# Kernel tuning notes

Measured on AMD Instinct MI355X. Metric: run time of the kernel, lower is better.

Reference implementation:

```python
import jax, jax.numpy as jnp
import numpy as np

MASS = 1.0
CHARGE = 1.0
LX = 10.0
LY = 10.0
COUPLING = 1.0
NPER = 1  # module hardcodes self.nper = 1


def _periodic_internal_energy(xy):
    """Sum over 9 periodic image shifts of masked Coulomb energy.

    Mirrors MovingPoints.periodic_internal_energy / dislocated_internal_energy:
    for each (n, m) in {-1,0,1}^2, dists = cdist(xy, xy + [n*lx, m*ly]) with an
    +inf diagonal mask (so diagonal contributes 0 after 1/d), energy += sum(c*q^2/d).
    """
    n = xy.shape[0]
    eye = jnp.eye(n, dtype=bool)
    # pairwise coordinate differences, [N, N]
    dx = xy[:, None, 0] - xy[None, :, 0]
    dy = xy[:, None, 1] - xy[None, :, 1]
    cq2 = COUPLING * CHARGE ** 2
    energy = jnp.zeros((), dtype=xy.dtype)
    shifts = [(i * LX, j * LY) for i in range(-NPER, NPER + 1) for j in range(-NPER, NPER + 1)]
    for sx, sy in shifts:
        # cdist(xy, xy + shift): d_ij = ||xy_i - xy_j - shift||
        d2 = (dx - sx) ** 2 + (dy - sy) ** 2
        # diagonal masked with +inf in original -> 1/d = 0 on diagonal;
        # use where with a safe distance so forward is identical and grads are clean.
        d = jnp.sqrt(jnp.where(eye, 1.0, d2))
        energy = energy + jnp.sum(jnp.where(eye, 0.0, cq2 / d))
    return energy


def setup_inputs() -> dict:
    key = jax.random.key(0)
    k1, k2 = jax.random.split(key)
    N = 8192
    # positions uniform in the periodic box [0, LX] x [0, LY]
    xy = jax.random.uniform(k1, (N, 2), dtype=jnp.float32) * jnp.array([LX, LY], dtype=jnp.float32)
    pxy = jax.random.normal(k2, (N, 2), dtype=jnp.float32)
    return {"xy": xy, "pxy": pxy}


def reference(xy, pxy):
    # hamiltonian = kinetic_energy(pxy) + potential_energy_(xy) with no external objects
    ke = jnp.sum(pxy ** 2) / (2.0 * MASS)
    pe = _periodic_internal_energy(xy)
    return ke + pe
```

## Files before the change

### kernel.cpp

```cpp
#include <hip/hip_runtime.h>

#define N 8192

#define BGRID 64
#define BINV 6.4f
#define NBINS (BGRID * BGRID)
#define FDIM 127
#define FSIZE (FDIM * FDIM)
#define FH 0.15625f

#define RC2 0.25f
#define GA 3.75f
#define GB (-10.0f)
#define GC 12.0f

#define CELLG 20
#define CELLINV 2.0f
#define NCELLS (CELLG * CELLG)
#define CAP 64
#define SRCAP 384

#define FBLOCKS 64
#define HISTBLOCKS 4
#define KEBLOCKS 8
#define BUILDBLOCKS 8
#define NCORR 512

#define WS_F 0
#define WS_HIST 16384
#define WS_CELLN 32768
#define WS_CELLS 33280
#define WS_CORR 84480
#define WS_SR 84992
#define WS_KE 85504

#define RSQ __builtin_amdgcn_rsqf

__global__ __launch_bounds__(256) void prep_kernel(const float* __restrict__ xy,
                                                   const float* __restrict__ pxy,
                                                   float* __restrict__ F,
                                                   unsigned* __restrict__ hist,
                                                   float* __restrict__ ke_part,
                                                   unsigned* __restrict__ cell_n,
                                                   float2* __restrict__ cells) {
    const int t = threadIdx.x;
    const int b = blockIdx.x;
    if (b < FBLOCKS) {
        int k = b * 256 + t;
        if (k < FSIZE) {
            float a  = (float)(k % FDIM - 63) * FH;
            float bb = (float)(k / FDIM - 63) * FH;
            int ixm = (__builtin_fabsf(a)  <= 5.0f) ? 0 : (a  > 0.0f ? -1 : 1);
            int iym = (__builtin_fabsf(bb) <= 5.0f) ? 0 : (bb > 0.0f ? -1 : 1);
            float s = 0.0f;
            for (int iy = -1; iy <= 1; ++iy)
                for (int ix = -1; ix <= 1; ++ix) {
                    if (ix == ixm && iy == iym) continue;
                    float xs = __builtin_fmaf(10.0f, (float)ix, a);
                    float ys = __builtin_fmaf(10.0f, (float)iy, bb);
                    s += RSQ(xs * xs + ys * ys);
                }
            float ux = 5.0f - __builtin_fabsf(__builtin_fabsf(a) - 5.0f);
            float uy = 5.0f - __builtin_fabsf(__builtin_fabsf(bb) - 5.0f);
            float r2 = __builtin_fmaf(uy, uy, ux * ux);
            float gcap = (r2 >= RC2)
                       ? RSQ(r2)
                       : __builtin_fmaf(__builtin_fmaf(GC, r2, GB), r2, GA);
            F[k] = s + gcap;
        }
    } else if (b < FBLOCKS + HISTBLOCKS) {
        __shared__ unsigned lh[NBINS];
        const int hb = b - FBLOCKS;
        for (int k = t; k < NBINS; k += 256) lh[k] = 0u;
        __syncthreads();
        const float2* p2 = (const float2*)xy;
        for (int r = 0; r < 8; ++r) {
            float2 p = p2[hb * 2048 + r * 256 + t];
            int cx = (int)(p.x * BINV); cx = cx > 63 ? 63 : cx;
            int cy = (int)(p.y * BINV); cy = cy > 63 ? 63 : cy;
            atomicAdd(&lh[cy * BGRID + cx], 1u);
        }
        __syncthreads();
        for (int k = t; k < NBINS; k += 256) hist[hb * NBINS + k] = lh[k];
    } else if (b < FBLOCKS + HISTBLOCKS + KEBLOCKS) {
        const int kb = b - FBLOCKS - HISTBLOCKS;
        const float4* p4 = (const float4*)pxy;
        float acc = 0.0f;
        for (int k = kb * 256 + t; k < (2 * N) / 4; k += KEBLOCKS * 256) {
            float4 v = p4[k];
            acc += 0.5f * (v.x * v.x + v.y * v.y + v.z * v.z + v.w * v.w);
        }
        for (int off = 32; off > 0; off >>= 1)
            acc += __shfl_down(acc, off, 64);
        __shared__ float ws[4];
        if ((t & 63) == 0) ws[t >> 6] = acc;
        __syncthreads();
        if (t == 0) ke_part[kb] = (ws[0] + ws[1]) + (ws[2] + ws[3]);
    } else {
        const int pb = b - FBLOCKS - HISTBLOCKS - KEBLOCKS;
        const float2* p2 = (const float2*)xy;
        for (int k = pb * 1024 + t; k < pb * 1024 + 1024; k += 256) {
            float2 p = p2[k];
            int cx = (int)(p.x * CELLINV); cx = cx > CELLG - 1 ? CELLG - 1 : cx;
            int cy = (int)(p.y * CELLINV); cy = cy > CELLG - 1 ? CELLG - 1 : cy;
            int c = cy * CELLG + cx;
            unsigned slot = atomicAdd(&cell_n[c], 1u);
            if (slot < CAP) cells[c * CAP + slot] = p;
        }
    }
}

__global__ __launch_bounds__(128) void main_kernel(const float* __restrict__ F,
                                                   const unsigned* __restrict__ hist,
                                                   const unsigned* __restrict__ cell_n,
                                                   const float2* __restrict__ cells,
                                                   float* __restrict__ corr_part,
                                                   float* __restrict__ sr_part) {
    const int t = threadIdx.x;
    __shared__ float smem[1664];
    __shared__ float wsum[2];

    if (blockIdx.x < NCORR) {
        float (*corrF)[128] = (float (*)[128])smem;
        float (*corrN)[64]  = (float (*)[64])(smem + 1024);
        const int cid = blockIdx.x;
        const int y1 = cid >> 3;
        const int y2b = (cid & 7) * 8;
        const int x1 = t & 63;
        const int x2c = t >> 6;
        const int x2base = x2c * 32;
#pragma unroll
        for (int s = 0; s < 8; ++s) {
            if (t < FDIM)
                corrF[s][t] = F[(y1 - (y2b + s) + 63) * FDIM + t];
            if (t < 64) {
                int hi = (y2b + s) * BGRID + t;
                corrN[s][t] = (float)(hist[hi] + hist[NBINS + hi]
                                    + hist[2 * NBINS + hi] + hist[3 * NBINS + hi]);
            }
        }
        int h1 = y1 * BGRID + x1;
        float n1 = (float)(hist[h1] + hist[NBINS + h1]
                         + hist[2 * NBINS + h1] + hist[3 * NBINS + h1]);
        __syncthreads();
        const int fb = 63 + x1 - x2base;
        float acc = 0.0f;
#pragma unroll
        for (int s = 0; s < 8; ++s) {
            const float* Fr = &corrF[s][0];
            const float* Nr = &corrN[s][x2base];
            float sum = 0.0f;
#pragma unroll 8
            for (int k = 0; k < 32; ++k)
                sum = __builtin_fmaf(Nr[k], Fr[fb - k], sum);
            acc += sum;
        }
        acc *= n1;
        for (int off = 32; off > 0; off >>= 1)
            acc += __shfl_down(acc, off, 64);
        if ((t & 63) == 0) wsum[t >> 6] = acc;
        __syncthreads();
        if (t == 0) corr_part[cid] = wsum[0] + wsum[1];
        return;
    }

    float* spx  = smem;
    float* spy  = smem + 384;
    int*   stag = (int*)(smem + 768);

    const int c  = blockIdx.x - NCORR;
    const int cx = c % CELLG, cy = c / CELLG;

    const int offs[9][2] = {{0,0},{-1,-1},{0,-1},{1,-1},{-1,0},{1,0},{-1,1},{0,1},{1,1}};
    int base = 0, n0 = 0;
#pragma unroll
    for (int nn = 0; nn < 9; ++nn) {
        int cx2 = cx + offs[nn][0];
        cx2 += (cx2 < 0) ? CELLG : 0;  cx2 -= (cx2 >= CELLG) ? CELLG : 0;
        int cy2 = cy + offs[nn][1];
        cy2 += (cy2 < 0) ? CELLG : 0;  cy2 -= (cy2 >= CELLG) ? CELLG : 0;
        int cc = cy2 * CELLG + cx2;
        int len = (int)cell_n[cc];  len = len > CAP ? CAP : len;
        if (nn == 0) n0 = len;
        for (int k = t; k < len; k += 128) {
            int d = base + k;
            if (d < SRCAP) {
                float2 q = cells[cc * CAP + k];
                spx[d] = q.x;  spy[d] = q.y;  stag[d] = cc * CAP + k;
            }
        }
        base += len;
    }
    const int M = base > SRCAP ? SRCAP : base;
    __syncthreads();

    float acc = 0.0f;
    for (int i = 0; i < n0; ++i) {
        float pxi = spx[i], pyi = spy[i];
        int itag = c * CAP + i;
        for (int j = t; j < M; j += 128) {
            float dx = pxi - spx[j];
            float dy = pyi - spy[j];
            float ux = 5.0f - __builtin_fabsf(__builtin_fabsf(dx) - 5.0f);
            float uy = 5.0f - __builtin_fabsf(__builtin_fabsf(dy) - 5.0f);
            float s2 = __builtin_fmaf(uy, uy, ux * ux);
            float v = RSQ(s2) - __builtin_fmaf(__builtin_fmaf(GC, s2, GB), s2, GA);
            bool ok = (s2 < RC2) && (stag[j] != itag);
            acc += ok ? v : 0.0f;
        }
    }
    for (int off = 32; off > 0; off >>= 1)
        acc += __shfl_down(acc, off, 64);
    if ((t & 63) == 0) wsum[t >> 6] = acc;
    __syncthreads();
    if (t == 0) sr_part[c] = wsum[0] + wsum[1];
}

__global__ __launch_bounds__(1024) void finish_kernel(const float* __restrict__ corr_part,
                                                      const float* __restrict__ sr_part,
                                                      const float* __restrict__ ke_part,
                                                      const float* __restrict__ F,
                                                      float* __restrict__ out) {
    const int t = threadIdx.x;
    float acc = 0.0f;
    if (t < NCORR) acc += corr_part[t];
    if (t < NCELLS) acc += sr_part[t];
    if (t < KEBLOCKS) acc += ke_part[t];
    if (t == 0) acc -= (float)N * F[63 * FDIM + 63];
    for (int off = 32; off > 0; off >>= 1)
        acc += __shfl_down(acc, off, 64);
    __shared__ float ws[16];
    if ((t & 63) == 0) ws[t >> 6] = acc;
    __syncthreads();
    if (t == 0) {
        float s = 0.0f;
        for (int w = 0; w < 16; ++w) s += ws[w];
        out[0] = s;
    }
}

extern "C" void kernel_launch(void* const* d_in, const int* in_sizes, int n_in,
                              void* d_out, int out_size, void* d_ws, size_t ws_size,
                              hipStream_t stream) {
    const float* xy  = (const float*)d_in[0];
    const float* pxy = (const float*)d_in[1];
    float* out       = (float*)d_out;
    float* wsf       = (float*)d_ws;
    float* F         = wsf + WS_F;
    unsigned* hist   = (unsigned*)(wsf + WS_HIST);
    unsigned* cell_n = (unsigned*)(wsf + WS_CELLN);
    float2* cells    = (float2*)(wsf + WS_CELLS);
    float* corr_part = wsf + WS_CORR;
    float* sr_part   = wsf + WS_SR;
    float* ke_part   = wsf + WS_KE;

    hipMemsetAsync(cell_n, 0, NCELLS * sizeof(unsigned), stream);
    prep_kernel<<<FBLOCKS + HISTBLOCKS + KEBLOCKS + BUILDBLOCKS, 256, 0, stream>>>(
        xy, pxy, F, hist, ke_part, cell_n, cells);
    main_kernel<<<NCORR + NCELLS, 128, 0, stream>>>(
        F, hist, cell_n, cells, corr_part, sr_part);
    finish_kernel<<<1, 1024, 0, stream>>>(corr_part, sr_part, ke_part, F, out);
}
```

Before: 32.20 us.

## Build cell lists per slice in shared memory and drop the memset launch

The cell-binning step now gives each build block its own per-cell slice, counted with shared-memory atomics instead of global atomics. Per-slice counts are written to global memory, so the separate hipMemsetAsync that zeroed counters is no longer needed. The short-range blocks gather 72 segments through a prefix sum and a binary search, and take the self-exclusion tag from the stored source index. This removes one launch and global atomic contention, at the cost of more gather logic and a per-slice capacity of 24 that could overflow for dense cells.

```diff
diff --git a/kernel.cpp b/kernel.cpp
--- a/kernel.cpp
+++ b/kernel.cpp
@@ -17,22 +17,22 @@
 #define CELLG 20
 #define CELLINV 2.0f
 #define NCELLS (CELLG * CELLG)
-#define CAP 64
+#define NSLICE 8
+#define CAPS 24
 #define SRCAP 384
 
 #define FBLOCKS 64
 #define HISTBLOCKS 4
 #define KEBLOCKS 8
-#define BUILDBLOCKS 8
 #define NCORR 512
 
 #define WS_F 0
 #define WS_HIST 16384
-#define WS_CELLN 32768
-#define WS_CELLS 33280
-#define WS_CORR 84480
-#define WS_SR 84992
-#define WS_KE 85504
+#define WS_CNT 32768
+#define WS_CELLS 36864
+#define WS_CORR 190464
+#define WS_SR 190976
+#define WS_KE 191488
 
 #define RSQ __builtin_amdgcn_rsqf
 
@@ -41,7 +41,7 @@
                                                    float* __restrict__ F,
                                                    unsigned* __restrict__ hist,
                                                    float* __restrict__ ke_part,
-                                                   unsigned* __restrict__ cell_n,
+                                                   unsigned* __restrict__ cnt_g,
                                                    float2* __restrict__ cells) {
     const int t = threadIdx.x;
     const int b = blockIdx.x;
@@ -97,22 +97,27 @@
         __syncthreads();
         if (t == 0) ke_part[kb] = (ws[0] + ws[1]) + (ws[2] + ws[3]);
     } else {
+        __shared__ unsigned cur[NCELLS];
         const int pb = b - FBLOCKS - HISTBLOCKS - KEBLOCKS;
         const float2* p2 = (const float2*)xy;
-        for (int k = pb * 1024 + t; k < pb * 1024 + 1024; k += 256) {
-            float2 p = p2[k];
+        for (int k = t; k < NCELLS; k += 256) cur[k] = 0u;
+        __syncthreads();
+        for (int r = 0; r < 4; ++r) {
+            float2 p = p2[pb * 1024 + r * 256 + t];
             int cx = (int)(p.x * CELLINV); cx = cx > CELLG - 1 ? CELLG - 1 : cx;
             int cy = (int)(p.y * CELLINV); cy = cy > CELLG - 1 ? CELLG - 1 : cy;
             int c = cy * CELLG + cx;
-            unsigned slot = atomicAdd(&cell_n[c], 1u);
-            if (slot < CAP) cells[c * CAP + slot] = p;
-        }
+            unsigned slot = atomicAdd(&cur[c], 1u);
+            if (slot < CAPS) cells[(c * NSLICE + pb) * CAPS + slot] = p;
+        }
+        __syncthreads();
+        for (int k = t; k < NCELLS; k += 256) cnt_g[k * NSLICE + pb] = cur[k];
     }
 }
 
 __global__ __launch_bounds__(128) void main_kernel(const float* __restrict__ F,
                                                    const unsigned* __restrict__ hist,
-                                                   const unsigned* __restrict__ cell_n,
+                                                   const unsigned* __restrict__ cnt_g,
                                                    const float2* __restrict__ cells,
                                                    float* __restrict__ corr_part,
                                                    float* __restrict__ sr_part) {
@@ -164,40 +169,56 @@
         return;
     }
 
-    float* spx  = smem;
-    float* spy  = smem + 384;
-    int*   stag = (int*)(smem + 768);
+    float* spx      = smem;
+    float* spy      = smem + 384;
+    int*   stag     = (int*)(smem + 768);
+    int*   segbase  = (int*)(smem + 1152);
+    unsigned* seglen = (unsigned*)(smem + 1225);
+    int*   cc9      = (int*)(smem + 1297);
 
     const int c  = blockIdx.x - NCORR;
     const int cx = c % CELLG, cy = c / CELLG;
 
-    const int offs[9][2] = {{0,0},{-1,-1},{0,-1},{1,-1},{-1,0},{1,0},{-1,1},{0,1},{1,1}};
-    int base = 0, n0 = 0;
-#pragma unroll
-    for (int nn = 0; nn < 9; ++nn) {
-        int cx2 = cx + offs[nn][0];
+    if (t < 9) {
+        const int ox[9] = {0,-1,0,1,-1,1,-1,0,1};
+        const int oy[9] = {0,-1,-1,-1,0,0,1,1,1};
+        int cx2 = cx + ox[t];
         cx2 += (cx2 < 0) ? CELLG : 0;  cx2 -= (cx2 >= CELLG) ? CELLG : 0;
-        int cy2 = cy + offs[nn][1];
+        int cy2 = cy + oy[t];
         cy2 += (cy2 < 0) ? CELLG : 0;  cy2 -= (cy2 >= CELLG) ? CELLG : 0;
-        int cc = cy2 * CELLG + cx2;
-        int len = (int)cell_n[cc];  len = len > CAP ? CAP : len;
-        if (nn == 0) n0 = len;
-        for (int k = t; k < len; k += 128) {
-            int d = base + k;
-            if (d < SRCAP) {
-                float2 q = cells[cc * CAP + k];
-                spx[d] = q.x;  spy[d] = q.y;  stag[d] = cc * CAP + k;
-            }
-        }
-        base += len;
-    }
-    const int M = base > SRCAP ? SRCAP : base;
+        cc9[t] = cy2 * CELLG + cx2;
+    }
+    __syncthreads();
+    if (t < 72) {
+        unsigned L = cnt_g[cc9[t >> 3] * NSLICE + (t & 7)];
+        seglen[t] = L > CAPS ? CAPS : L;
+    }
+    __syncthreads();
+    if (t < 73) {
+        int b2 = 0;
+        for (int j = 0; j < t; ++j) b2 += (int)seglen[j];
+        segbase[t] = b2;
+    }
+    __syncthreads();
+    const int n0 = segbase[8];
+    int M = segbase[72];  M = M > SRCAP ? SRCAP : M;
+
+    for (int g = t; g < M; g += 128) {
+        int lo = 0, hi = 71;
+        while (lo < hi) {
+            int mid = (lo + hi + 1) >> 1;
+            if (segbase[mid] <= g) lo = mid; else hi = mid - 1;
+        }
+        int src = (cc9[lo >> 3] * NSLICE + (lo & 7)) * CAPS + (g - segbase[lo]);
+        float2 q = cells[src];
+        spx[g] = q.x;  spy[g] = q.y;  stag[g] = src;
+    }
     __syncthreads();
 
     float acc = 0.0f;
     for (int i = 0; i < n0; ++i) {
         float pxi = spx[i], pyi = spy[i];
-        int itag = c * CAP + i;
+        int itag = stag[i];
         for (int j = t; j < M; j += 128) {
             float dx = pxi - spx[j];
             float dy = pyi - spy[j];
@@ -248,16 +269,15 @@
     float* wsf       = (float*)d_ws;
     float* F         = wsf + WS_F;
     unsigned* hist   = (unsigned*)(wsf + WS_HIST);
-    unsigned* cell_n = (unsigned*)(wsf + WS_CELLN);
+    unsigned* cnt_g  = (unsigned*)(wsf + WS_CNT);
     float2* cells    = (float2*)(wsf + WS_CELLS);
     float* corr_part = wsf + WS_CORR;
     float* sr_part   = wsf + WS_SR;
     float* ke_part   = wsf + WS_KE;
 
-    hipMemsetAsync(cell_n, 0, NCELLS * sizeof(unsigned), stream);
-    prep_kernel<<<FBLOCKS + HISTBLOCKS + KEBLOCKS + BUILDBLOCKS, 256, 0, stream>>>(
-        xy, pxy, F, hist, ke_part, cell_n, cells);
+    prep_kernel<<<FBLOCKS + HISTBLOCKS + KEBLOCKS + NSLICE, 256, 0, stream>>>(
+        xy, pxy, F, hist, ke_part, cnt_g, cells);
     main_kernel<<<NCORR + NCELLS, 128, 0, stream>>>(
-        F, hist, cell_n, cells, corr_part, sr_part);
+        F, hist, cnt_g, cells, corr_part, sr_part);
     finish_kernel<<<1, 1024, 0, stream>>>(corr_part, sr_part, ke_part, F, out);
 }
```

Result: faster. 27.39 us (-14.9%).

## Fuse prep into main kernel with per-block redundant histogram and neighbor gather

Applied to the files above, without the earlier changes.

Removes the memset and prep kernel. Each correlation block now rebuilds the full 64x64 histogram in shared memory and computes its F rows inline, and each short-range block scans all points to gather its 3x3 neighborhood. Kinetic energy moves into the finish kernel. This trades two launches and global round-trips for much redundant work: 912 blocks each read all 8192 points and do shared atomics.

```diff
diff --git a/kernel.cpp b/kernel.cpp
--- a/kernel.cpp
+++ b/kernel.cpp
@@ -6,7 +6,6 @@
 #define BINV 6.4f
 #define NBINS (BGRID * BGRID)
 #define FDIM 127
-#define FSIZE (FDIM * FDIM)
 #define FH 0.15625f
 
 #define RC2 0.25f
@@ -17,138 +16,82 @@
 #define CELLG 20
 #define CELLINV 2.0f
 #define NCELLS (CELLG * CELLG)
-#define CAP 64
 #define SRCAP 384
 
-#define FBLOCKS 64
-#define HISTBLOCKS 4
-#define KEBLOCKS 8
-#define BUILDBLOCKS 8
 #define NCORR 512
-
-#define WS_F 0
-#define WS_HIST 16384
-#define WS_CELLN 32768
-#define WS_CELLS 33280
-#define WS_CORR 84480
-#define WS_SR 84992
-#define WS_KE 85504
+#define NBLK (NCORR + NCELLS)
+
+#define WS_CORR 0
+#define WS_SR 512
 
 #define RSQ __builtin_amdgcn_rsqf
 
-__global__ __launch_bounds__(256) void prep_kernel(const float* __restrict__ xy,
-                                                   const float* __restrict__ pxy,
-                                                   float* __restrict__ F,
-                                                   unsigned* __restrict__ hist,
-                                                   float* __restrict__ ke_part,
-                                                   unsigned* __restrict__ cell_n,
-                                                   float2* __restrict__ cells) {
-    const int t = threadIdx.x;
-    const int b = blockIdx.x;
-    if (b < FBLOCKS) {
-        int k = b * 256 + t;
-        if (k < FSIZE) {
-            float a  = (float)(k % FDIM - 63) * FH;
-            float bb = (float)(k / FDIM - 63) * FH;
-            int ixm = (__builtin_fabsf(a)  <= 5.0f) ? 0 : (a  > 0.0f ? -1 : 1);
-            int iym = (__builtin_fabsf(bb) <= 5.0f) ? 0 : (bb > 0.0f ? -1 : 1);
-            float s = 0.0f;
-            for (int iy = -1; iy <= 1; ++iy)
-                for (int ix = -1; ix <= 1; ++ix) {
-                    if (ix == ixm && iy == iym) continue;
-                    float xs = __builtin_fmaf(10.0f, (float)ix, a);
-                    float ys = __builtin_fmaf(10.0f, (float)iy, bb);
-                    s += RSQ(xs * xs + ys * ys);
-                }
-            float ux = 5.0f - __builtin_fabsf(__builtin_fabsf(a) - 5.0f);
-            float uy = 5.0f - __builtin_fabsf(__builtin_fabsf(bb) - 5.0f);
-            float r2 = __builtin_fmaf(uy, uy, ux * ux);
-            float gcap = (r2 >= RC2)
-                       ? RSQ(r2)
-                       : __builtin_fmaf(__builtin_fmaf(GC, r2, GB), r2, GA);
-            F[k] = s + gcap;
-        }
-    } else if (b < FBLOCKS + HISTBLOCKS) {
-        __shared__ unsigned lh[NBINS];
-        const int hb = b - FBLOCKS;
-        for (int k = t; k < NBINS; k += 256) lh[k] = 0u;
-        __syncthreads();
-        const float2* p2 = (const float2*)xy;
-        for (int r = 0; r < 8; ++r) {
-            float2 p = p2[hb * 2048 + r * 256 + t];
-            int cx = (int)(p.x * BINV); cx = cx > 63 ? 63 : cx;
-            int cy = (int)(p.y * BINV); cy = cy > 63 ? 63 : cy;
-            atomicAdd(&lh[cy * BGRID + cx], 1u);
-        }
-        __syncthreads();
-        for (int k = t; k < NBINS; k += 256) hist[hb * NBINS + k] = lh[k];
-    } else if (b < FBLOCKS + HISTBLOCKS + KEBLOCKS) {
-        const int kb = b - FBLOCKS - HISTBLOCKS;
-        const float4* p4 = (const float4*)pxy;
-        float acc = 0.0f;
-        for (int k = kb * 256 + t; k < (2 * N) / 4; k += KEBLOCKS * 256) {
-            float4 v = p4[k];
-            acc += 0.5f * (v.x * v.x + v.y * v.y + v.z * v.z + v.w * v.w);
-        }
-        for (int off = 32; off > 0; off >>= 1)
-            acc += __shfl_down(acc, off, 64);
-        __shared__ float ws[4];
-        if ((t & 63) == 0) ws[t >> 6] = acc;
-        __syncthreads();
-        if (t == 0) ke_part[kb] = (ws[0] + ws[1]) + (ws[2] + ws[3]);
-    } else {
-        const int pb = b - FBLOCKS - HISTBLOCKS - KEBLOCKS;
-        const float2* p2 = (const float2*)xy;
-        for (int k = pb * 1024 + t; k < pb * 1024 + 1024; k += 256) {
-            float2 p = p2[k];
-            int cx = (int)(p.x * CELLINV); cx = cx > CELLG - 1 ? CELLG - 1 : cx;
-            int cy = (int)(p.y * CELLINV); cy = cy > CELLG - 1 ? CELLG - 1 : cy;
-            int c = cy * CELLG + cx;
-            unsigned slot = atomicAdd(&cell_n[c], 1u);
-            if (slot < CAP) cells[c * CAP + slot] = p;
-        }
-    }
-}
-
-__global__ __launch_bounds__(128) void main_kernel(const float* __restrict__ F,
-                                                   const unsigned* __restrict__ hist,
-                                                   const unsigned* __restrict__ cell_n,
-                                                   const float2* __restrict__ cells,
+__device__ __forceinline__ float Fnode(float a, float bb) {
+    int ixm = (__builtin_fabsf(a)  <= 5.0f) ? 0 : (a  > 0.0f ? -1 : 1);
+    int iym = (__builtin_fabsf(bb) <= 5.0f) ? 0 : (bb > 0.0f ? -1 : 1);
+    float s = 0.0f;
+    for (int iy = -1; iy <= 1; ++iy)
+        for (int ix = -1; ix <= 1; ++ix) {
+            if (ix == ixm && iy == iym) continue;
+            float xs = __builtin_fmaf(10.0f, (float)ix, a);
+            float ys = __builtin_fmaf(10.0f, (float)iy, bb);
+            s += RSQ(xs * xs + ys * ys);
+        }
+    float ux = 5.0f - __builtin_fabsf(__builtin_fabsf(a) - 5.0f);
+    float uy = 5.0f - __builtin_fabsf(__builtin_fabsf(bb) - 5.0f);
+    float r2 = __builtin_fmaf(uy, uy, ux * ux);
+    float gcap = (r2 >= RC2) ? RSQ(r2)
+                             : __builtin_fmaf(__builtin_fmaf(GC, r2, GB), r2, GA);
+    return s + gcap;
+}
+
+__global__ __launch_bounds__(128) void main_kernel(const float* __restrict__ xy,
                                                    float* __restrict__ corr_part,
                                                    float* __restrict__ sr_part) {
     const int t = threadIdx.x;
-    __shared__ float smem[1664];
+    const int b = blockIdx.x;
+    __shared__ unsigned arena[5632];
     __shared__ float wsum[2];
-
-    if (blockIdx.x < NCORR) {
-        float (*corrF)[128] = (float (*)[128])smem;
-        float (*corrN)[64]  = (float (*)[64])(smem + 1024);
-        const int cid = blockIdx.x;
-        const int y1 = cid >> 3;
-        const int y2b = (cid & 7) * 8;
+    const float4* __restrict__ xy4 = (const float4*)xy;
+
+    if (b < NCORR) {
+        unsigned* lh = arena;
+        float (*rowF)[128] = (float (*)[128])(arena + 4096);
+        float (*rowN)[64]  = (float (*)[64])(arena + 5120);
+
+        for (int k = t; k < NBINS; k += 128) lh[k] = 0u;
+        __syncthreads();
+        for (int i = t; i < 4096; i += 128) {
+            float4 v = xy4[i];
+            int cx0 = (int)(v.x * BINV); cx0 = cx0 > 63 ? 63 : cx0;
+            int cy0 = (int)(v.y * BINV); cy0 = cy0 > 63 ? 63 : cy0;
+            atomicAdd(&lh[cy0 * BGRID + cx0], 1u);
+            int cx1 = (int)(v.z * BINV); cx1 = cx1 > 63 ? 63 : cx1;
+            int cy1 = (int)(v.w * BINV); cy1 = cy1 > 63 ? 63 : cy1;
+            atomicAdd(&lh[cy1 * BGRID + cx1], 1u);
+        }
+
+        const int y1 = b >> 3;
+        const int y2b = (b & 7) * 8;
+#pragma unroll
+        for (int s = 0; s < 8; ++s)
+            if (t < FDIM)
+                rowF[s][t] = Fnode((float)(t - 63) * FH, (float)(y1 - y2b - s) * FH);
+        __syncthreads();
+
+        for (int k = t; k < 512; k += 128)
+            rowN[k >> 6][k & 63] = (float)lh[(y2b + (k >> 6)) * BGRID + (k & 63)];
+        __syncthreads();
+
         const int x1 = t & 63;
-        const int x2c = t >> 6;
-        const int x2base = x2c * 32;
-#pragma unroll
-        for (int s = 0; s < 8; ++s) {
-            if (t < FDIM)
-                corrF[s][t] = F[(y1 - (y2b + s) + 63) * FDIM + t];
-            if (t < 64) {
-                int hi = (y2b + s) * BGRID + t;
-                corrN[s][t] = (float)(hist[hi] + hist[NBINS + hi]
-                                    + hist[2 * NBINS + hi] + hist[3 * NBINS + hi]);
-            }
-        }
-        int h1 = y1 * BGRID + x1;
-        float n1 = (float)(hist[h1] + hist[NBINS + h1]
-                         + hist[2 * NBINS + h1] + hist[3 * NBINS + h1]);
-        __syncthreads();
+        const int x2base = (t >> 6) * 32;
         const int fb = 63 + x1 - x2base;
+        float n1 = (float)lh[y1 * BGRID + x1];
         float acc = 0.0f;
 #pragma unroll
         for (int s = 0; s < 8; ++s) {
-            const float* Fr = &corrF[s][0];
-            const float* Nr = &corrN[s][x2base];
+            const float* Fr = &rowF[s][0];
+            const float* Nr = &rowN[s][x2base];
             float sum = 0.0f;
 #pragma unroll 8
             for (int k = 0; k < 32; ++k)
@@ -160,44 +103,52 @@
             acc += __shfl_down(acc, off, 64);
         if ((t & 63) == 0) wsum[t >> 6] = acc;
         __syncthreads();
-        if (t == 0) corr_part[cid] = wsum[0] + wsum[1];
+        if (t == 0) corr_part[b] = wsum[0] + wsum[1];
         return;
     }
 
-    float* spx  = smem;
-    float* spy  = smem + 384;
-    int*   stag = (int*)(smem + 768);
-
-    const int c  = blockIdx.x - NCORR;
+    float* spx     = (float*)arena;
+    float* spy     = (float*)(arena + 384);
+    int*   stag    = (int*)(arena + 768);
+    int*   sown    = (int*)(arena + 1152);
+    unsigned* cur  = arena + 1216;
+
+    const int c  = b - NCORR;
     const int cx = c % CELLG, cy = c / CELLG;
-
-    const int offs[9][2] = {{0,0},{-1,-1},{0,-1},{1,-1},{-1,0},{1,0},{-1,1},{0,1},{1,1}};
-    int base = 0, n0 = 0;
+    if (t < 2) cur[t] = 0u;
+    __syncthreads();
+
+    for (int i = t; i < 4096; i += 128) {
+        float4 v = xy4[i];
 #pragma unroll
-    for (int nn = 0; nn < 9; ++nn) {
-        int cx2 = cx + offs[nn][0];
-        cx2 += (cx2 < 0) ? CELLG : 0;  cx2 -= (cx2 >= CELLG) ? CELLG : 0;
-        int cy2 = cy + offs[nn][1];
-        cy2 += (cy2 < 0) ? CELLG : 0;  cy2 -= (cy2 >= CELLG) ? CELLG : 0;
-        int cc = cy2 * CELLG + cx2;
-        int len = (int)cell_n[cc];  len = len > CAP ? CAP : len;
-        if (nn == 0) n0 = len;
-        for (int k = t; k < len; k += 128) {
-            int d = base + k;
-            if (d < SRCAP) {
-                float2 q = cells[cc * CAP + k];
-                spx[d] = q.x;  spy[d] = q.y;  stag[d] = cc * CAP + k;
+        for (int h = 0; h < 2; ++h) {
+            float px = h ? v.z : v.x;
+            float py = h ? v.w : v.y;
+            int cx2 = (int)(px * CELLINV); cx2 = cx2 > CELLG - 1 ? CELLG - 1 : cx2;
+            int cy2 = (int)(py * CELLINV); cy2 = cy2 > CELLG - 1 ? CELLG - 1 : cy2;
+            int ddx = cx2 - cx;  ddx += (ddx < -CELLG/2) ? CELLG : 0;  ddx -= (ddx > CELLG/2) ? CELLG : 0;
+            int ddy = cy2 - cy;  ddy += (ddy < -CELLG/2) ? CELLG : 0;  ddy -= (ddy > CELLG/2) ? CELLG : 0;
+            if (ddx >= -1 && ddx <= 1 && ddy >= -1 && ddy <= 1) {
+                unsigned m = atomicAdd(&cur[0], 1u);
+                if (m < SRCAP) {
+                    spx[m] = px;  spy[m] = py;  stag[m] = 2 * i + h;
+                    if (ddx == 0 && ddy == 0) {
+                        unsigned o = atomicAdd(&cur[1], 1u);
+                        if (o < 64) sown[o] = (int)m;
+                    }
+                }
             }
         }
-        base += len;
-    }
-    const int M = base > SRCAP ? SRCAP : base;
-    __syncthreads();
+    }
+    __syncthreads();
+    int M  = (int)cur[0];  M  = M  > SRCAP ? SRCAP : M;
+    int n0 = (int)cur[1];  n0 = n0 > 64 ? 64 : n0;
 
     float acc = 0.0f;
-    for (int i = 0; i < n0; ++i) {
+    for (int oi = 0; oi < n0; ++oi) {
+        int i = sown[oi];
         float pxi = spx[i], pyi = spy[i];
-        int itag = c * CAP + i;
+        int itag = stag[i];
         for (int j = t; j < M; j += 128) {
             float dx = pxi - spx[j];
             float dy = pyi - spy[j];
@@ -218,15 +169,18 @@
 
 __global__ __launch_bounds__(1024) void finish_kernel(const float* __restrict__ corr_part,
                                                       const float* __restrict__ sr_part,
-                                                      const float* __restrict__ ke_part,
-                                                      const float* __restrict__ F,
+                                                      const float* __restrict__ pxy,
                                                       float* __restrict__ out) {
     const int t = threadIdx.x;
     float acc = 0.0f;
     if (t < NCORR) acc += corr_part[t];
     if (t < NCELLS) acc += sr_part[t];
-    if (t < KEBLOCKS) acc += ke_part[t];
-    if (t == 0) acc -= (float)N * F[63 * FDIM + 63];
+    const float4* p4 = (const float4*)pxy;
+    for (int k = t; k < (2 * N) / 4; k += 1024) {
+        float4 v = p4[k];
+        acc += 0.5f * (v.x * v.x + v.y * v.y + v.z * v.z + v.w * v.w);
+    }
+    if (t == 0) acc -= (float)N * Fnode(0.0f, 0.0f);
     for (int off = 32; off > 0; off >>= 1)
         acc += __shfl_down(acc, off, 64);
     __shared__ float ws[16];
@@ -246,18 +200,9 @@
     const float* pxy = (const float*)d_in[1];
     float* out       = (float*)d_out;
     float* wsf       = (float*)d_ws;
-    float* F         = wsf + WS_F;
-    unsigned* hist   = (unsigned*)(wsf + WS_HIST);
-    unsigned* cell_n = (unsigned*)(wsf + WS_CELLN);
-    float2* cells    = (float2*)(wsf + WS_CELLS);
     float* corr_part = wsf + WS_CORR;
     float* sr_part   = wsf + WS_SR;
-    float* ke_part   = wsf + WS_KE;
-
-    hipMemsetAsync(cell_n, 0, NCELLS * sizeof(unsigned), stream);
-    prep_kernel<<<FBLOCKS + HISTBLOCKS + KEBLOCKS + BUILDBLOCKS, 256, 0, stream>>>(
-        xy, pxy, F, hist, ke_part, cell_n, cells);
-    main_kernel<<<NCORR + NCELLS, 128, 0, stream>>>(
-        F, hist, cell_n, cells, corr_part, sr_part);
-    finish_kernel<<<1, 1024, 0, stream>>>(corr_part, sr_part, ke_part, F, out);
-}
+
+    main_kernel<<<NBLK, 128, 0, stream>>>(xy, corr_part, sr_part);
+    finish_kernel<<<1, 1024, 0, stream>>>(corr_part, sr_part, pxy, out);
+}
```

After: 35.18 us. +9.3%, slower.
